# Optimization experiments

Measured on AMD Instinct MI355X. Metric: run time of the kernel, lower is better.

The kernel has to match this reference:

```python
import jax, jax.numpy as jnp
import numpy as np

# Ordered bi-bi mechanism, species order per _build_species_list:
# [E, EA, EQ, EAB, A, B, P, Q] -> indices 0..7
# Transitions: E+A<->EA, EA+B<->EAB, EAB<->EQ+P, EQ<->E+Q (all reversible)
N_SPECIES = 8
N_TRANS = 4

# forward: rate * [enzyme] * prod([substrates]); -1 = no factor (padded)
ENZ_F = np.array([0, 1, 3, 2], dtype=np.int32)          # E, EA, EAB, EQ
SUB_F = np.array([[4], [5], [-1], [-1]], dtype=np.int32)  # A, B, -, -
# reverse: rate * [to-enzyme] * prod([products])
ENZ_R = np.array([1, 3, 2, 0], dtype=np.int32)          # EA, EAB, EQ, E
PROD_R = np.array([[-1], [-1], [6], [7]], dtype=np.int32)  # -, -, P, Q
REV_MASK = np.array([1.0, 1.0, 1.0, 1.0], dtype=np.float32)

# Stoichiometry (n_trans, n_species), applied as dydt += v_net[:,None]*S[i]
S_FORWARD = np.array([
    [-1,  1,  0,  0, -1,  0,  0,  0],
    [ 0, -1,  0,  1,  0, -1,  0,  0],
    [ 0,  0,  1, -1,  0,  0,  1,  0],
    [ 1,  0, -1,  0,  0,  0,  0,  1],
], dtype=np.float32)


def _masked_gather_prod(y, idx):
    # y: (B, n_species); idx: (n_trans, k) with -1 padding
    safe = jnp.maximum(idx, 0)
    g = y[:, safe.reshape(-1)].reshape(y.shape[0], idx.shape[0], idx.shape[1])  # (B,T,k)
    g = jnp.where(idx[None, :, :] >= 0, g, 1.0)
    return jnp.prod(g, axis=-1)  # (B, T)


def setup_inputs() -> dict:
    key = jax.random.key(0)
    k1, k2, k3 = jax.random.split(key, 3)
    B = 2_000_000
    return {
        "t": jnp.zeros((1,), dtype=jnp.float32),
        "y": jax.random.uniform(k1, (B, N_SPECIES), dtype=jnp.float32),
        "forward_rates": jax.random.uniform(k2, (B, N_TRANS), dtype=jnp.float32),
        "reverse_rates": jax.random.uniform(k3, (B, N_TRANS), dtype=jnp.float32),
    }


def reference(t, y, forward_rates, reverse_rates):
    enz_f = jnp.asarray(ENZ_F)
    enz_r = jnp.asarray(ENZ_R)
    sub_f = jnp.asarray(SUB_F)
    prod_r = jnp.asarray(PROD_R)
    S = jnp.asarray(S_FORWARD)
    rev_mask = jnp.asarray(REV_MASK)

    # v_forward[b,i] = k_f[b,i] * y[b, enz_f[i]] * prod_j y[b, sub_f[i,j]]
    v_f = forward_rates * y[:, enz_f] * _masked_gather_prod(y, sub_f)
    # v_reverse analogous, zeroed for irreversible transitions
    v_r = reverse_rates * y[:, enz_r] * _masked_gather_prod(y, prod_r) * rev_mask[None, :]
    v_net = v_f - v_r  # (B, T)
    # dydt[b,s] = sum_i v_net[b,i] * S[i,s]
    return jnp.einsum("bt,ts->bs", v_net, S)
```

## Files before the change

### kernel.cpp

```cpp
#include <hip/hip_runtime.h>


#define ITERS 4

__device__ __forceinline__ float4 shfl_xor1(float4 v) {
    float4 r;
    r.x = __shfl_xor(v.x, 1);
    r.y = __shfl_xor(v.y, 1);
    r.z = __shfl_xor(v.z, 1);
    r.w = __shfl_xor(v.w, 1);
    return r;
}

__device__ __forceinline__ float4 ode_compute(float4 q, float4 mine, int h) {
    float4 p = shfl_xor1(q);
    float4 ya = h ? p : q;
    float4 yb = h ? q : p;

    float4 other = shfl_xor1(mine);
    float4 f = h ? other : mine;
    float4 r = h ? mine : other;

    float E  = ya.x, EA = ya.y, EQ = ya.z, EAB = ya.w;
    float A  = yb.x, Bc = yb.y, P  = yb.z, Q   = yb.w;

    float v0 = f.x * E   * A  - r.x * EA;
    float v1 = f.y * EA  * Bc - r.y * EAB;
    float v2 = f.z * EAB      - r.z * EQ * P;
    float v3 = f.w * EQ       - r.w * E  * Q;

    float4 o;
    if (h == 0) {
        o.x = v3 - v0;
        o.y = v0 - v1;
        o.z = v2 - v3;
        o.w = v1 - v2;
    } else {
        o.x = -v0;
        o.y = -v1;
        o.z =  v2;
        o.w =  v3;
    }
    return o;
}

__global__ __launch_bounds__(256) void ode_kernel(
    const float4* __restrict__ y4,
    const float4* __restrict__ kf4,
    const float4* __restrict__ kr4,
    float4* __restrict__ out4,
    int n2)
{
    const int stride = gridDim.x * blockDim.x;
    const int t0 = blockIdx.x * blockDim.x + threadIdx.x;
    const int h = t0 & 1;

    const float4* __restrict__ rp = h ? kr4 : kf4;

    if (t0 + (ITERS - 1) * stride < n2) {
        float4 q[ITERS], mine[ITERS];
        #pragma unroll
        for (int k = 0; k < ITERS; ++k) {
            int t = t0 + k * stride;
            q[k]    = y4[t];
            mine[k] = rp[t >> 1];
        }

        float4 o[ITERS];
        #pragma unroll
        for (int k = 0; k < ITERS; ++k)
            o[k] = ode_compute(q[k], mine[k], h);

        #pragma unroll
        for (int k = 0; k < ITERS; ++k)
            out4[t0 + k * stride] = o[k];
    } else {
        #pragma unroll
        for (int k = 0; k < ITERS; ++k) {
            int t = t0 + k * stride;
            if (t < n2) {
                float4 q    = y4[t];
                float4 mine = rp[t >> 1];
                out4[t] = ode_compute(q, mine, h);
            }
        }
    }
}

extern "C" void kernel_launch(void* const* d_in, const int* in_sizes, int n_in,
                              void* d_out, int out_size, void* d_ws, size_t ws_size,
                              hipStream_t stream) {
    const float4* y4  = (const float4*)d_in[1];
    const float4* kf4 = (const float4*)d_in[2];
    const float4* kr4 = (const float4*)d_in[3];
    float4* out4 = (float4*)d_out;
    int B  = in_sizes[1] / 8;
    int n2 = 2 * B;

    int block = 256;
    int grid  = (n2 + block * ITERS - 1) / (block * ITERS);
    ode_kernel<<<grid, block, 0, stream>>>(y4, kf4, kr4, out4, n2);
}
```

Baseline: 174.5 us.

## Use persistent grid-stride loop with one-ahead register prefetch

Replaces the fixed four-way unrolled batch per thread with a persistent grid of at most 2048 blocks. Each thread walks a grid-stride loop and loads the next element while computing and storing the current one. Launch bounds now request 8 blocks per CU. The aim is to cut launch and tail overhead and keep loads in flight steadily, but only one load is outstanding ahead per thread, which may expose less memory parallelism than four independent loads.

```diff
diff --git a/kernel.cpp b/kernel.cpp
--- a/kernel.cpp
+++ b/kernel.cpp
@@ -1,7 +1,5 @@
 #include <hip/hip_runtime.h>
 
-
-#define ITERS 4
 
 __device__ __forceinline__ float4 shfl_xor1(float4 v) {
     float4 r;
@@ -44,46 +42,39 @@
     return o;
 }
 
-__global__ __launch_bounds__(256) void ode_kernel(
+__global__ __launch_bounds__(256, 8) void ode_kernel(
     const float4* __restrict__ y4,
     const float4* __restrict__ kf4,
     const float4* __restrict__ kr4,
     float4* __restrict__ out4,
     int n2)
 {
-    const int stride = gridDim.x * blockDim.x;
-    const int t0 = blockIdx.x * blockDim.x + threadIdx.x;
-    const int h = t0 & 1;
+    const int T  = gridDim.x * blockDim.x;
+    int t = blockIdx.x * blockDim.x + threadIdx.x;
+    const int h = t & 1;
 
     const float4* __restrict__ rp = h ? kr4 : kf4;
 
-    if (t0 + (ITERS - 1) * stride < n2) {
-        float4 q[ITERS], mine[ITERS];
-        #pragma unroll
-        for (int k = 0; k < ITERS; ++k) {
-            int t = t0 + k * stride;
-            q[k]    = y4[t];
-            mine[k] = rp[t >> 1];
+    bool v = t < n2;
+    float4 q, m;
+    if (v) {
+        q = y4[t];
+        m = rp[t >> 1];
+    }
+
+    while (v) {
+        int  tn = t + T;
+        bool vn = tn < n2;
+        float4 qn, mn;
+        if (vn) {
+            qn = y4[tn];
+            mn = rp[tn >> 1];
         }
 
-        float4 o[ITERS];
-        #pragma unroll
-        for (int k = 0; k < ITERS; ++k)
-            o[k] = ode_compute(q[k], mine[k], h);
+        float4 o = ode_compute(q, m, h);
+        out4[t] = o;
 
-        #pragma unroll
-        for (int k = 0; k < ITERS; ++k)
-            out4[t0 + k * stride] = o[k];
-    } else {
-        #pragma unroll
-        for (int k = 0; k < ITERS; ++k) {
-            int t = t0 + k * stride;
-            if (t < n2) {
-                float4 q    = y4[t];
-                float4 mine = rp[t >> 1];
-                out4[t] = ode_compute(q, mine, h);
-            }
-        }
+        t = tn; v = vn; q = qn; m = mn;
     }
 }
 
@@ -98,6 +89,8 @@
     int n2 = 2 * B;
 
     int block = 256;
-    int grid  = (n2 + block * ITERS - 1) / (block * ITERS);
+    int grid  = 2048;
+    int maxg  = (n2 + block - 1) / block;
+    if (grid > maxg) grid = maxg;
     ode_kernel<<<grid, block, 0, stream>>>(y4, kf4, kr4, out4, n2);
 }
```

Result: no change. 175.4 us (+0.5%).
